# Performance work log

Measured on AMD Instinct MI355X. Metric: run time of the kernel, lower is better.

The kernel has to match this reference:

```python
import jax, jax.numpy as jnp
import numpy as np

N = 100000
E = 1600000
F_IN = 32   # node_features
F_H = 32    # filters
F_OUT = 4


def setup_inputs() -> dict:
    key = jax.random.key(0)
    ks = jax.random.split(key, 24)
    inp = {
        'x': jax.random.normal(ks[0], (N, F_IN), dtype=jnp.float32),
        'edge_index': jax.random.randint(ks[1], (2, E), 0, N, dtype=jnp.int64),
        'edge_weight': jax.random.uniform(ks[2], (E,), dtype=jnp.float32),
        'H': jax.random.normal(ks[3], (N, F_H), dtype=jnp.float32),
    }
    # ChebConv params: W[k] for k in {0,1} (K=2), bias per conv.
    def cheb_params(kw, kb, fin):
        s = 1.0 / np.sqrt(fin)
        W = jax.random.uniform(kw, (2, fin, F_H), jnp.float32, -s, s)
        b = jax.random.uniform(kb, (F_H,), jnp.float32, -s, s)
        return W, b
    names = ['xz', 'hz', 'xr', 'hr', 'xh', 'hh']
    fins = [F_IN, F_H, F_IN, F_H, F_IN, F_H]
    for i, (nm, fin) in enumerate(zip(names, fins)):
        W, b = cheb_params(ks[4 + 2 * i], ks[5 + 2 * i], fin)
        inp['W' + nm] = W
        inp['b' + nm] = b
    s = 1.0 / np.sqrt(F_H)
    inp['lin_w'] = jax.random.uniform(ks[20], (F_H, F_OUT), jnp.float32, -s, s)
    inp['lin_b'] = jax.random.uniform(ks[21], (F_OUT,), jnp.float32, -s, s)
    return inp


def _cheb(x, src, dst, nw, W, b):
    # ChebConv, K=2, sym norm, lambda_max=2 => L_hat = -D^{-1/2} A D^{-1/2}
    # (diagonal of scaled Laplacian cancels exactly: 1 - 1 = 0).
    tx1 = -jax.ops.segment_sum(nw[:, None] * x[src], dst, num_segments=N)
    return x @ W[0] + tx1 @ W[1] + b


def reference(x, edge_index, edge_weight, H,
              Wxz, bxz, Whz, bhz, Wxr, bxr, Whr, bhr, Wxh, bxh, Whh, bhh,
              lin_w, lin_b):
    src, dst = edge_index[0], edge_index[1]
    # remove_self_loops equivalent: zero out self-loop weights
    w = jnp.where(src == dst, 0.0, edge_weight)
    deg = jax.ops.segment_sum(w, src, num_segments=N)
    dinv = jnp.where(deg > 0, jax.lax.rsqrt(jnp.maximum(deg, 1e-30)), 0.0)
    nw = dinv[src] * w * dinv[dst]  # per-edge sym-normalized weight

    Z = jax.nn.sigmoid(_cheb(x, src, dst, nw, Wxz, bxz) +
                       _cheb(H, src, dst, nw, Whz, bhz))
    R = jax.nn.sigmoid(_cheb(x, src, dst, nw, Wxr, bxr) +
                       _cheb(H, src, dst, nw, Whr, bhr))
    H_tilde = jnp.tanh(_cheb(x, src, dst, nw, Wxh, bxh) +
                       _cheb(H * R, src, dst, nw, Whh, bhh))
    h = Z * H + (1.0 - Z) * H_tilde
    out = jax.nn.relu(h) @ lin_w + lin_b
    return (out, h)
```

## Files before the change

kernel.cpp:

```cpp
#include <hip/hip_runtime.h>
#include <hip/hip_bf16.h>
#include <hip/hip_fp16.h>

typedef __hip_bfloat16 bf16;
typedef __attribute__((ext_vector_type(8))) short bf16x8;
typedef __attribute__((ext_vector_type(4))) float f32x4;

#define NN   100000
#define EE   1600000
#define FH   32
#define FOUT 4
#define NBD  782
#define NBS  196
#define CAPB 2432
#define CAPS 8960
#define CAP  64
#define BINBLK 256
#define BINTHR 1024
#define EPB  6250
#define MFMA16(a, b, c) __builtin_amdgcn_mfma_f32_16x16x32_bf16(a, b, c, 0, 0, 0)

__device__ __forceinline__ float b2f(bf16 v) { return __bfloat162float(v); }

__device__ __forceinline__ float ldf(const void* p, int i, int f32) {
    return f32 ? ((const float*)p)[i] : b2f(((const bf16*)p)[i]);
}
__device__ __forceinline__ int ldi(const void* p, int i, int i64f) {
    return i64f ? (int)(((const long long*)p)[i]) : ((const int*)p)[i];
}
__device__ __forceinline__ void stf(void* p, int i, int f32, float v) {
    if (f32) ((float*)p)[i] = v;
    else     ((bf16*)p)[i] = __float2bfloat16(v);
}
__device__ __forceinline__ float h2f(unsigned short u) {
    return __half2float(__ushort_as_half(u));
}
__device__ __forceinline__ unsigned short f2h16(float v) {
    return __half_as_ushort(__float2half(v));
}
__device__ __forceinline__ short f2bf(float v) {
    unsigned u = __float_as_uint(v);
    return (short)((u + 0x7FFFu + ((u >> 16) & 1u)) >> 16);
}
__device__ __forceinline__ unsigned q8(float v) {
    int q = (int)rintf(v * 16.f) + 128;
    q = q < 0 ? 0 : (q > 255 ? 255 : q);
    return (unsigned)q;
}
__device__ __forceinline__ float ub(unsigned w, int k) {
    return (float)((w >> (k * 8)) & 0xFFu);
}
__device__ __forceinline__ float4 bfly_g(float4 v) {
    v.x += __shfl_xor(v.x, 8);  v.y += __shfl_xor(v.y, 8);
    v.z += __shfl_xor(v.z, 8);  v.w += __shfl_xor(v.w, 8);
    v.x += __shfl_xor(v.x, 16); v.y += __shfl_xor(v.y, 16);
    v.z += __shfl_xor(v.z, 16); v.w += __shfl_xor(v.w, 16);
    return v;
}
__device__ __forceinline__ bf16x8 bfragT(const short* __restrict__ wt, int idx) {
    return *(const bf16x8*)(wt + idx);
}

__global__ __launch_bounds__(256) void k_prep(
    const void* __restrict__ x, const void* __restrict__ H,
    const void* __restrict__ ei,
    const void* __restrict__ W0, const void* __restrict__ W1,
    const void* __restrict__ W2, const void* __restrict__ W3,
    const void* __restrict__ W4, const void* __restrict__ W5,
    int* __restrict__ flg, int* __restrict__ binCur, int* __restrict__ binCurS,
    short* __restrict__ wt, unsigned* __restrict__ xh,
    unsigned short* __restrict__ xh8) {
    __shared__ int s_fl[2];
    int t = threadIdx.x, b = blockIdx.x;
    if (t == 0) { s_fl[0] = 0; s_fl[1] = 0; }
    __syncthreads();
    {
        float v = b2f(((const bf16*)x)[t]);
        if ((!isfinite(v)) || (fabsf(v) > 100.f)) atomicOr(&s_fl[0], 1);
        int w32 = ((const int*)ei)[t];
        if ((t & 1) && (w32 != 0)) atomicOr(&s_fl[1], 1);
    }
    __syncthreads();
    int f32 = s_fl[0];
    int i64 = s_fl[1] ? 0 : 1;
    if (b == 0 && t == 0) { flg[0] = f32; flg[1] = i64; }
    if (b < 48) {
        int i = b * 256 + t;
        int mat = i >> 11;
        int r = i & 2047;
        int cheb = r >> 10, k = (r >> 5) & 31, n = r & 31;
        const void* W = (mat == 0) ? W0 : (mat == 1) ? W1 : (mat == 2) ? W2
                      : (mat == 3) ? W3 : (mat == 4) ? W4 : W5;
        wt[(((mat << 1) + cheb) << 10) + n * 32 + k] = f2bf(ldf(W, r, f32));
    } else if (b == 48) {
        for (int i = t; i < NBD; i += 256) binCur[i] = i * CAPB;
    } else if (b == 49) {
        for (int i = t; i < NBS; i += 256) binCurS[i] = i * CAPS;
    }
    int i = b * 256 + t;
    if (i < NN * FH) {
        float xv = ldf(x, i, f32);
        float hv = ldf(H, i, f32);
        xh[i] = ((unsigned)f2h16(hv) << 16) | f2h16(xv);
        xh8[i] = (unsigned short)((q8(hv) << 8) | q8(xv));
    }
}

__global__ __launch_bounds__(BINTHR) void k_bin(const void* __restrict__ ei,
                                                const void* __restrict__ ew,
                                                const int* __restrict__ flg,
                                                int* __restrict__ binCur,
                                                int* __restrict__ binCurS,
                                                int2* __restrict__ dstRec,
                                                int* __restrict__ srcRec) {
    __shared__ int hD[NBD], bD[NBD], lofD[NBD];
    __shared__ int hS[NBS], bS[NBS], lofS[NBS];
    __shared__ int sWave[16];
    __shared__ int2 stD[EPB];
    __shared__ int  stS[EPB];
    int t = threadIdx.x;
    int lane = t & 63, wv = t >> 6;
    for (int i = t; i < NBD; i += BINTHR) hD[i] = 0;
    for (int i = t; i < NBS; i += BINTHR) hS[i] = 0;
    __syncthreads();
    int e0 = blockIdx.x * EPB;
    int e1 = e0 + EPB; if (e1 > EE) e1 = EE;
    int f32 = flg[0], i64 = flg[1];
    for (int e = e0 + t; e < e1; e += BINTHR) {
        int s = ldi(ei, e, i64);
        int d = ldi(ei, EE + e, i64);
        atomicAdd(&hD[d >> 7], 1);
        atomicAdd(&hS[s >> 9], 1);
    }
    __syncthreads();
    for (int i = t; i < NBD; i += BINTHR)
        bD[i] = (hD[i] > 0) ? atomicAdd(&binCur[i], hD[i]) : 0;
    for (int i = t; i < NBS; i += BINTHR)
        bS[i] = (hS[i] > 0) ? atomicAdd(&binCurS[i], hS[i]) : 0;
    int vD = (t < NBD) ? hD[t] : 0;
    int p = vD;
    #pragma unroll
    for (int ofs = 1; ofs < 64; ofs <<= 1) {
        int u = __shfl_up(p, ofs);
        if (lane >= ofs) p += u;
    }
    if (lane == 63) sWave[wv] = p;
    __syncthreads();
    if (t < 16) {
        int q = sWave[t];
        #pragma unroll
        for (int ofs = 1; ofs < 16; ofs <<= 1) {
            int u = __shfl_up(q, ofs);
            if (t >= ofs) q += u;
        }
        sWave[t] = q;
    }
    __syncthreads();
    if (t < NBD) {
        int incl = p + (wv ? sWave[wv - 1] : 0);
        lofD[t] = incl - vD;
        hD[t] = 0;
    }
    __syncthreads();
    int vS = (t < NBS) ? hS[t] : 0;
    p = vS;
    #pragma unroll
    for (int ofs = 1; ofs < 64; ofs <<= 1) {
        int u = __shfl_up(p, ofs);
        if (lane >= ofs) p += u;
    }
    if (lane == 63) sWave[wv] = p;
    __syncthreads();
    if (t < 16) {
        int q = sWave[t];
        #pragma unroll
        for (int ofs = 1; ofs < 16; ofs <<= 1) {
            int u = __shfl_up(q, ofs);
            if (t >= ofs) q += u;
        }
        sWave[t] = q;
    }
    __syncthreads();
    if (t < NBS) {
        int incl = p + (wv ? sWave[wv - 1] : 0);
        lofS[t] = incl - vS;
        hS[t] = 0;
    }
    __syncthreads();
    for (int e = e0 + t; e < e1; e += BINTHR) {
        int s = ldi(ei, e, i64);
        int d = ldi(ei, EE + e, i64);
        float w = (s == d) ? 0.f : ldf(ew, e, f32);
        int wh = (int)(f2h16(w) & 0x7FFFu);
        int bd = d >> 7, bs = s >> 9;
        int rd = atomicAdd(&hD[bd], 1);
        int rs = atomicAdd(&hS[bs], 1);
        stD[lofD[bd] + rd] = make_int2((int)(((unsigned)s << 15) | wh),
                                       (bd << 8) | (d & 127));
        stS[lofS[bs] + rs] = (int)(((unsigned)bs << 24) |
                                   ((unsigned)(s & 511) << 15) | (unsigned)wh);
    }
    __syncthreads();
    int tot = e1 - e0;
    for (int i = t; i < tot; i += BINTHR) {
        int2 r = stD[i];
        int bin = ((unsigned)r.y) >> 8;
        int g = bD[bin] + (i - lofD[bin]);
        if (g < (bin + 1) * CAPB) dstRec[g] = make_int2(r.x, r.y & 127);
        int u = stS[i];
        int sbin = ((unsigned)u) >> 24;
        int gs = bS[sbin] + (i - lofS[sbin]);
        if (gs < (sbin + 1) * CAPS) srcRec[gs] = u & 0xFFFFFF;
    }
}

__global__ __launch_bounds__(256) void k_degb(const int* __restrict__ binCurS,
                                              const int* __restrict__ srcRec,
                                              float* __restrict__ dinv) {
    __shared__ float lDeg[512];
    int b = blockIdx.x, t = threadIdx.x;
    lDeg[t] = 0.f; lDeg[t + 256] = 0.f;
    __syncthreads();
    int cnt = binCurS[b] - b * CAPS;
    if (cnt > CAPS) cnt = CAPS;
    for (int i = t; i < cnt; i += 256) {
        int r = srcRec[b * CAPS + i];
        atomicAdd(&lDeg[(r >> 15) & 511], h2f((unsigned short)(r & 0x7FFF)));
    }
    __syncthreads();
    #pragma unroll
    for (int k = 0; k < 2; k++) {
        int li = t + k * 256;
        int node = b * 512 + li;
        if (node < NN) {
            float dv = lDeg[li];
            dinv[node] = (dv > 0.f) ? rsqrtf(dv) : 0.f;
        }
    }
}

__global__ __launch_bounds__(256) void k_fgz(
    const int* __restrict__ binCur, const int2* __restrict__ dstRec,
    const float* __restrict__ dinv, const unsigned short* __restrict__ xh8,
    const unsigned* __restrict__ xh, const int* __restrict__ flg,
    const short* __restrict__ wt,
    const void* __restrict__ bxz, const void* __restrict__ bhz,
    const void* __restrict__ bxr, const void* __restrict__ bhr,
    int* __restrict__ cursor, int* __restrict__ ell,
    unsigned* __restrict__ axah, unsigned short* __restrict__ zf16,
    unsigned short* __restrict__ hr16) {
    __shared__ int lCur[128];
    __shared__ int lEll[128 * CAP];
    __shared__ unsigned sAX[128][33];
    int b = blockIdx.x, t = threadIdx.x;
    if (t < 128) lCur[t] = 0;
    __syncthreads();
    int cnt = binCur[b] - b * CAPB;
    if (cnt > CAPB) cnt = CAPB;
    for (int i = t; i < cnt; i += 256) {
        int2 r = dstRec[b * CAPB + i];
        int slot = atomicAdd(&lCur[r.y], 1);
        if (slot < CAP) lEll[r.y * CAP + slot] = r.x;
    }
    __syncthreads();
    int nodeBase = b * 128;
    for (int i = t; i < 128 * CAP; i += 256) {
        int node = nodeBase + (i >> 6);
        if (node < NN && (i & 63) < lCur[i >> 6])
            ell[(size_t)node * CAP + (i & 63)] = lEll[i];
    }
    if (t < 128 && nodeBase + t < NN) {
        int c2 = lCur[t]; if (c2 > CAP) c2 = CAP;
        cursor[nodeBase + t] = c2;
    }
    int gg = t >> 5, f = t & 31, g = f >> 3, c = f & 7;
    for (int pass = 0; pass < 16; pass++) {
        int ln = pass * 8 + gg;
        int node = nodeBase + ln;
        if (node >= NN) continue;
        int cnt2 = lCur[ln]; if (cnt2 > CAP) cnt2 = CAP;
        int base = ln * CAP;
        float4 ax = {0.f, 0.f, 0.f, 0.f}, ah = {0.f, 0.f, 0.f, 0.f};
        float cs = 0.f;
        for (int j = 0; j < cnt2; j += 16) {
            int wrd[4]; float cf[4]; uint2 pv[4];
            #pragma unroll
            for (int u = 0; u < 4; u++) {
                int jj = j + u * 4 + g;
                wrd[u] = (jj < cnt2) ? lEll[base + jj] : 0;
            }
            #pragma unroll
            for (int u = 0; u < 4; u++) {
                int s = ((unsigned)wrd[u]) >> 15;
                cf[u] = dinv[s] * h2f((unsigned short)(wrd[u] & 0x7FFF));
                pv[u] = ((const uint2*)xh8)[s * 8 + c];
            }
            #pragma unroll
            for (int u = 0; u < 4; u++) {
                cs += cf[u];
                ax.x += cf[u] * ub(pv[u].x, 0);
                ah.x += cf[u] * ub(pv[u].x, 1);
                ax.y += cf[u] * ub(pv[u].x, 2);
                ah.y += cf[u] * ub(pv[u].x, 3);
                ax.z += cf[u] * ub(pv[u].y, 0);
                ah.z += cf[u] * ub(pv[u].y, 1);
                ax.w += cf[u] * ub(pv[u].y, 2);
                ah.w += cf[u] * ub(pv[u].y, 3);
            }
        }
        ax = bfly_g(ax); ah = bfly_g(ah);
        cs += __shfl_xor(cs, 8);
        cs += __shfl_xor(cs, 16);
        if (g == 0) {
            float dd = -dinv[node];
            float bias = 8.f * cs;
            uint4 o;
            o.x = ((unsigned)f2h16(dd * (ah.x * 0.0625f - bias)) << 16)
                | f2h16(dd * (ax.x * 0.0625f - bias));
            o.y = ((unsigned)f2h16(dd * (ah.y * 0.0625f - bias)) << 16)
                | f2h16(dd * (ax.y * 0.0625f - bias));
            o.z = ((unsigned)f2h16(dd * (ah.z * 0.0625f - bias)) << 16)
                | f2h16(dd * (ax.z * 0.0625f - bias));
            o.w = ((unsigned)f2h16(dd * (ah.w * 0.0625f - bias)) << 16)
                | f2h16(dd * (ax.w * 0.0625f - bias));
            sAX[ln][4 * c + 0] = o.x;
            sAX[ln][4 * c + 1] = o.y;
            sAX[ln][4 * c + 2] = o.z;
            sAX[ln][4 * c + 3] = o.w;
            ((uint4*)(axah + (size_t)node * FH))[c] = o;
        }
    }
    __syncthreads();
    int lane = t & 63, wv = t >> 6;
    int fl32 = flg[0];
    int cc = lane & 15, quad = lane >> 4, kb = quad * 8;
    float bz0 = ldf(bxz, cc, fl32) + ldf(bhz, cc, fl32);
    float bz1 = ldf(bxz, cc + 16, fl32) + ldf(bhz, cc + 16, fl32);
    float br0 = ldf(bxr, cc, fl32) + ldf(bhr, cc, fl32);
    float br1 = ldf(bxr, cc + 16, fl32) + ldf(bhr, cc + 16, fl32);
    for (int half = 0; half < 2; half++) {
        int nb2 = nodeBase + half * 64 + wv * 16;
        int nm = nb2 + cc; if (nm >= NN) nm = NN - 1;
        int lm = nm - nodeBase;
        bf16x8 fx, fHH, fAX, fAH;
        {
            const uint4* p = (const uint4*)(xh + (size_t)nm * FH + kb);
            uint4 aa = p[0], bb = p[1];
            unsigned wd[8] = {aa.x, aa.y, aa.z, aa.w, bb.x, bb.y, bb.z, bb.w};
            #pragma unroll
            for (int j = 0; j < 8; j++) {
                fx[j]  = f2bf(h2f((unsigned short)(wd[j] & 0xFFFF)));
                fHH[j] = f2bf(h2f((unsigned short)(wd[j] >> 16)));
            }
        }
        {
            unsigned wd[8];
            #pragma unroll
            for (int j = 0; j < 8; j++) wd[j] = sAX[lm][kb + j];
            #pragma unroll
            for (int j = 0; j < 8; j++) {
                fAX[j] = f2bf(h2f((unsigned short)(wd[j] & 0xFFFF)));
                fAH[j] = f2bf(h2f((unsigned short)(wd[j] >> 16)));
            }
        }
        f32x4 az0 = {bz0, bz0, bz0, bz0}, az1 = {bz1, bz1, bz1, bz1};
        f32x4 ar0 = {br0, br0, br0, br0}, ar1 = {br1, br1, br1, br1};
        int i0 = cc * 32 + kb;
        int i1 = (cc + 16) * 32 + kb;
        az0 = MFMA16(fx,  bfragT(wt, 0 * 1024 + i0), az0);
        az0 = MFMA16(fAX, bfragT(wt, 1 * 1024 + i0), az0);
        az0 = MFMA16(fHH, bfragT(wt, 2 * 1024 + i0), az0);
        az0 = MFMA16(fAH, bfragT(wt, 3 * 1024 + i0), az0);
        az1 = MFMA16(fx,  bfragT(wt, 0 * 1024 + i1), az1);
        az1 = MFMA16(fAX, bfragT(wt, 1 * 1024 + i1), az1);
        az1 = MFMA16(fHH, bfragT(wt, 2 * 1024 + i1), az1);
        az1 = MFMA16(fAH, bfragT(wt, 3 * 1024 + i1), az1);
        ar0 = MFMA16(fx,  bfragT(wt, 4 * 1024 + i0), ar0);
        ar0 = MFMA16(fAX, bfragT(wt, 5 * 1024 + i0), ar0);
        ar0 = MFMA16(fHH, bfragT(wt, 6 * 1024 + i0), ar0);
        ar0 = MFMA16(fAH, bfragT(wt, 7 * 1024 + i0), ar0);
        ar1 = MFMA16(fx,  bfragT(wt, 4 * 1024 + i1), ar1);
        ar1 = MFMA16(fAX, bfragT(wt, 5 * 1024 + i1), ar1);
        ar1 = MFMA16(fHH, bfragT(wt, 6 * 1024 + i1), ar1);
        ar1 = MFMA16(fAH, bfragT(wt, 7 * 1024 + i1), ar1);
        #pragma unroll
        for (int tl = 0; tl < 2; tl++) {
            f32x4 az = tl ? az1 : az0, ar = tl ? ar1 : ar0;
            int ff = cc + 16 * tl;
            #pragma unroll
            for (int r = 0; r < 4; r++) {
                int node = nb2 + quad * 4 + r;
                if (node < NN) {
                    float zv = 1.f / (1.f + expf(-az[r]));
                    float rv = 1.f / (1.f + expf(-ar[r]));
                    float Hv = h2f((unsigned short)(xh[(size_t)node * FH + ff] >> 16));
                    zf16[(size_t)node * FH + ff] = f2h16(zv);
                    hr16[(size_t)node * FH + ff] = f2h16(Hv * rv);
                }
            }
        }
    }
}

__global__ __launch_bounds__(256) void k_fgf(
    const int* __restrict__ cursor, const int* __restrict__ ell,
    const float* __restrict__ dinv, const unsigned short* __restrict__ hr16,
    const unsigned* __restrict__ xh, const unsigned* __restrict__ axah,
    const int* __restrict__ flg, const short* __restrict__ wt,
    const unsigned short* __restrict__ zf16,
    const void* __restrict__ bxh, const void* __restrict__ bhh,
    const void* __restrict__ lin_w, const void* __restrict__ lin_b,
    void* __restrict__ out) {
    __shared__ unsigned sAHR[64][17];
    __shared__ float srh[64][FH];
    __shared__ float slw[FH * FOUT];
    __shared__ float slb[FOUT];
    int b = blockIdx.x, t = threadIdx.x;
    int f32 = flg[0];
    if (t < FH * FOUT) slw[t] = ldf(lin_w, t, f32);
    if (t < FOUT) slb[t] = ldf(lin_b, t, f32);
    int nodeBase = b * 64;
    int gg = t >> 5, f = t & 31, g = f >> 3, c = f & 7;
    for (int pass = 0; pass < 8; pass++) {
        int ln = pass * 8 + gg;
        int node = nodeBase + ln;
        if (node >= NN) continue;
        int cnt = cursor[node];
        size_t base = (size_t)node * CAP;
        float4 acc = {0.f, 0.f, 0.f, 0.f};
        for (int j = 0; j < cnt; j += 16) {
            int wrd[4]; float cf[4]; ushort4 hv[4];
            #pragma unroll
            for (int u = 0; u < 4; u++) {
                int jj = j + u * 4 + g;
                wrd[u] = (jj < cnt) ? ell[base + jj] : 0;
            }
            #pragma unroll
            for (int u = 0; u < 4; u++) {
                int s = ((unsigned)wrd[u]) >> 15;
                cf[u] = dinv[s] * h2f((unsigned short)(wrd[u] & 0x7FFF));
                hv[u] = ((const ushort4*)hr16)[s * 8 + c];
            }
            #pragma unroll
            for (int u = 0; u < 4; u++) {
                acc.x += cf[u] * h2f(hv[u].x);
                acc.y += cf[u] * h2f(hv[u].y);
                acc.z += cf[u] * h2f(hv[u].z);
                acc.w += cf[u] * h2f(hv[u].w);
            }
        }
        acc = bfly_g(acc);
        if (g == 0) {
            float dd = -dinv[node];
            sAHR[ln][2 * c + 0] = ((unsigned)f2h16(dd * acc.y) << 16)
                                | f2h16(dd * acc.x);
            sAHR[ln][2 * c + 1] = ((unsigned)f2h16(dd * acc.w) << 16)
                                | f2h16(dd * acc.z);
        }
    }
    __syncthreads();
    int lane = t & 63, wv = t >> 6;
    int cc = lane & 15, quad = lane >> 4, kb = quad * 8;
    int nb2 = nodeBase + wv * 16;
    int nm = nb2 + cc; if (nm >= NN) nm = NN - 1;
    int lm = nm - nodeBase;
    bf16x8 fx, fAX, fHR, fAHR;
    {
        const uint4* p = (const uint4*)(xh + (size_t)nm * FH + kb);
        uint4 aa = p[0], bb = p[1];
        unsigned wd[8] = {aa.x, aa.y, aa.z, aa.w, bb.x, bb.y, bb.z, bb.w};
        #pragma unroll
        for (int j = 0; j < 8; j++)
            fx[j] = f2bf(h2f((unsigned short)(wd[j] & 0xFFFF)));
    }
    {
        const uint4* p = (const uint4*)(axah + (size_t)nm * FH + kb);
        uint4 aa = p[0], bb = p[1];
        unsigned wd[8] = {aa.x, aa.y, aa.z, aa.w, bb.x, bb.y, bb.z, bb.w};
        #pragma unroll
        for (int j = 0; j < 8; j++)
            fAX[j] = f2bf(h2f((unsigned short)(wd[j] & 0xFFFF)));
    }
    {
        const uint4* p = (const uint4*)(hr16 + (size_t)nm * FH + kb);
        uint4 aa = p[0];
        unsigned wd[4] = {aa.x, aa.y, aa.z, aa.w};
        #pragma unroll
        for (int j = 0; j < 8; j++)
            fHR[j] = f2bf(h2f((unsigned short)((wd[j >> 1] >> ((j & 1) * 16)) & 0xFFFF)));
    }
    {
        unsigned wd[4];
        #pragma unroll
        for (int m = 0; m < 4; m++) wd[m] = sAHR[lm][kb / 2 + m];
        #pragma unroll
        for (int j = 0; j < 8; j++)
            fAHR[j] = f2bf(h2f((unsigned short)((wd[j >> 1] >> ((j & 1) * 16)) & 0xFFFF)));
    }
    float bh0 = ldf(bxh, cc, f32) + ldf(bhh, cc, f32);
    float bh1 = ldf(bxh, cc + 16, f32) + ldf(bhh, cc + 16, f32);
    f32x4 a0 = {bh0, bh0, bh0, bh0}, a1 = {bh1, bh1, bh1, bh1};
    int i0 = cc * 32 + kb;
    int i1 = (cc + 16) * 32 + kb;
    a0 = MFMA16(fx,   bfragT(wt,  8 * 1024 + i0), a0);
    a0 = MFMA16(fAX,  bfragT(wt,  9 * 1024 + i0), a0);
    a0 = MFMA16(fHR,  bfragT(wt, 10 * 1024 + i0), a0);
    a0 = MFMA16(fAHR, bfragT(wt, 11 * 1024 + i0), a0);
    a1 = MFMA16(fx,   bfragT(wt,  8 * 1024 + i1), a1);
    a1 = MFMA16(fAX,  bfragT(wt,  9 * 1024 + i1), a1);
    a1 = MFMA16(fHR,  bfragT(wt, 10 * 1024 + i1), a1);
    a1 = MFMA16(fAHR, bfragT(wt, 11 * 1024 + i1), a1);
    #pragma unroll
    for (int tl = 0; tl < 2; tl++) {
        f32x4 a = tl ? a1 : a0;
        int ff = cc + 16 * tl;
        #pragma unroll
        for (int r = 0; r < 4; r++) {
            int node = nb2 + quad * 4 + r;
            if (node < NN) {
                float ht = tanhf(a[r]);
                float zv = h2f(zf16[(size_t)node * FH + ff]);
                float Hv = h2f((unsigned short)(xh[(size_t)node * FH + ff] >> 16));
                float hval = zv * Hv + (1.f - zv) * ht;
                stf(out, NN * FOUT + node * FH + ff, f32, hval);
                srh[node - nodeBase][ff] = hval > 0.f ? hval : 0.f;
            }
        }
    }
    __syncthreads();
    int nl = t >> 2, fo = t & 3;
    int node2 = nodeBase + nl;
    if (node2 < NN) {
        float acc = slb[fo];
        #pragma unroll
        for (int k = 0; k < FH; k++) acc += srh[nl][k] * slw[k * FOUT + fo];
        stf(out, node2 * FOUT + fo, f32, acc);
    }
}

extern "C" void kernel_launch(void* const* d_in, const int* in_sizes, int n_in,
                              void* d_out, int out_size, void* d_ws, size_t ws_size,
                              hipStream_t stream) {
    const void* x   = d_in[0];
    const void* ei  = d_in[1];
    const void* ew  = d_in[2];
    const void* H   = d_in[3];
    const void* Wxz = d_in[4];
    const void* bxz = d_in[5];
    const void* Whz = d_in[6];
    const void* bhz = d_in[7];
    const void* Wxr = d_in[8];
    const void* bxr = d_in[9];
    const void* Whr = d_in[10];
    const void* bhr = d_in[11];
    const void* Wxh = d_in[12];
    const void* bxh = d_in[13];
    const void* Whh = d_in[14];
    const void* bhh = d_in[15];
    const void* lnw = d_in[16];
    const void* lnb = d_in[17];

    char* base = (char*)d_ws;
    int*            flg     = (int*)base;            base += 64;
    int*            binCur  = (int*)base;            base += (NBD * 4 + 63) & ~63;
    int*            binCurS = (int*)base;            base += (NBS * 4 + 63) & ~63;
    float*          dinv    = (float*)base;          base += (size_t)NN * 4;
    int*            cursor  = (int*)base;            base += (size_t)NN * 4;
    short*          wt      = (short*)base;          base += (12288 * 2 + 63) & ~63;
    unsigned*       xh      = (unsigned*)base;       base += (size_t)NN * FH * 4;
    unsigned short* xh8     = (unsigned short*)base; base += (size_t)NN * FH * 2;
    unsigned*       axah    = (unsigned*)base;       base += (size_t)NN * FH * 4;
    unsigned short* zf16    = (unsigned short*)base; base += (size_t)NN * FH * 2;
    unsigned short* hr16    = (unsigned short*)base; base += (size_t)NN * FH * 2;
    int*            ell     = (int*)base;            base += (size_t)NN * CAP * 4;
    int2*           dstRec  = (int2*)base;           base += (size_t)NBD * CAPB * 8;
    int*            srcRec  = (int*)base;

    const int pb   = (NN * FH + 255) / 256;
    const int n64b = (NN + 63) / 64;

    k_prep<<<pb, 256, 0, stream>>>(x, H, ei, Wxz, Whz, Wxr, Whr, Wxh, Whh,
                                   flg, binCur, binCurS, wt, xh, xh8);
    k_bin<<<BINBLK, BINTHR, 0, stream>>>(ei, ew, flg, binCur, binCurS,
                                         dstRec, srcRec);
    k_degb<<<NBS, 256, 0, stream>>>(binCurS, srcRec, dinv);
    k_fgz<<<NBD, 256, 0, stream>>>(binCur, dstRec, dinv, xh8, xh, flg, wt,
                                   bxz, bhz, bxr, bhr,
                                   cursor, ell, axah, zf16, hr16);
    k_fgf<<<n64b, 256, 0, stream>>>(cursor, ell, dinv, hr16, xh, axah, flg, wt,
                                    zf16, bxh, bhh, lnw, lnb, d_out);
}
```

Measured before the change: 292.7 us.

## Split fused ELL-fill/gather/MFMA kernel into three separate kernels

Breaks the fused k_fgz kernel into three kernels: one that builds the ELL adjacency from binned records, one gather kernel with 8 nodes per block over many more blocks, and one MFMA kernel that computes the Z and R gates. The aim is more parallelism and occupancy for the gather, which previously used large shared memory and ran 16 serial passes per block. In exchange the gather now reads ELL from global memory instead of LDS, there are two extra kernel launches, and axah makes an extra round trip through global memory.

```diff
diff --git a/kernel.cpp b/kernel.cpp
--- a/kernel.cpp
+++ b/kernel.cpp
@@ -214,6 +214,35 @@
     }
 }
 
+__global__ __launch_bounds__(256) void k_fillb(const int* __restrict__ binCur,
+                                               const int2* __restrict__ dstRec,
+                                               int* __restrict__ cursor,
+                                               int* __restrict__ ell) {
+    __shared__ int lCur[128];
+    __shared__ int lEll[128 * CAP];
+    int b = blockIdx.x, t = threadIdx.x;
+    if (t < 128) lCur[t] = 0;
+    __syncthreads();
+    int cnt = binCur[b] - b * CAPB;
+    if (cnt > CAPB) cnt = CAPB;
+    for (int i = t; i < cnt; i += 256) {
+        int2 r = dstRec[b * CAPB + i];
+        int slot = atomicAdd(&lCur[r.y], 1);
+        if (slot < CAP) lEll[r.y * CAP + slot] = r.x;
+    }
+    __syncthreads();
+    int nodeBase = b * 128;
+    for (int i = t; i < 128 * CAP; i += 256) {
+        int node = nodeBase + (i >> 6);
+        if (node < NN && (i & 63) < lCur[i >> 6])
+            ell[(size_t)node * CAP + (i & (CAP - 1))] = lEll[i];
+    }
+    if (t < 128 && nodeBase + t < NN) {
+        int c = lCur[t]; if (c > CAP) c = CAP;
+        cursor[nodeBase + t] = c;
+    }
+}
+
 __global__ __launch_bounds__(256) void k_degb(const int* __restrict__ binCurS,
                                               const int* __restrict__ srcRec,
                                               float* __restrict__ dinv) {
@@ -239,164 +268,139 @@
     }
 }
 
-__global__ __launch_bounds__(256) void k_fgz(
-    const int* __restrict__ binCur, const int2* __restrict__ dstRec,
-    const float* __restrict__ dinv, const unsigned short* __restrict__ xh8,
-    const unsigned* __restrict__ xh, const int* __restrict__ flg,
-    const short* __restrict__ wt,
+__global__ __launch_bounds__(256) void k_gather1(const int* __restrict__ cursor,
+                                                 const int* __restrict__ ell,
+                                                 const float* __restrict__ dinv,
+                                                 const unsigned short* __restrict__ xh8,
+                                                 unsigned* __restrict__ axah) {
+    int t = threadIdx.x;
+    int node = blockIdx.x * 8 + (t >> 5);
+    if (node >= NN) return;
+    int f = t & 31;
+    int g = f >> 3, c = f & 7;
+    int cnt = cursor[node];
+    size_t base = (size_t)node * CAP;
+    float4 ax = {0.f, 0.f, 0.f, 0.f}, ah = {0.f, 0.f, 0.f, 0.f};
+    float cs = 0.f;
+    for (int j = 0; j < cnt; j += 16) {
+        int wrd[4]; float cf[4]; uint2 pv[4];
+        #pragma unroll
+        for (int u = 0; u < 4; u++) {
+            int jj = j + u * 4 + g;
+            wrd[u] = (jj < cnt) ? ell[base + jj] : 0;
+        }
+        #pragma unroll
+        for (int u = 0; u < 4; u++) {
+            int s = ((unsigned)wrd[u]) >> 15;
+            cf[u] = dinv[s] * h2f((unsigned short)(wrd[u] & 0x7FFF));
+            pv[u] = ((const uint2*)xh8)[s * 8 + c];
+        }
+        #pragma unroll
+        for (int u = 0; u < 4; u++) {
+            cs += cf[u];
+            ax.x += cf[u] * ub(pv[u].x, 0);
+            ah.x += cf[u] * ub(pv[u].x, 1);
+            ax.y += cf[u] * ub(pv[u].x, 2);
+            ah.y += cf[u] * ub(pv[u].x, 3);
+            ax.z += cf[u] * ub(pv[u].y, 0);
+            ah.z += cf[u] * ub(pv[u].y, 1);
+            ax.w += cf[u] * ub(pv[u].y, 2);
+            ah.w += cf[u] * ub(pv[u].y, 3);
+        }
+    }
+    ax = bfly_g(ax); ah = bfly_g(ah);
+    cs += __shfl_xor(cs, 8);
+    cs += __shfl_xor(cs, 16);
+    if (g == 0) {
+        float dd = -dinv[node];
+        float bias = 8.f * cs;
+        uint4 o;
+        o.x = ((unsigned)f2h16(dd * (ah.x * 0.0625f - bias)) << 16)
+            | f2h16(dd * (ax.x * 0.0625f - bias));
+        o.y = ((unsigned)f2h16(dd * (ah.y * 0.0625f - bias)) << 16)
+            | f2h16(dd * (ax.y * 0.0625f - bias));
+        o.z = ((unsigned)f2h16(dd * (ah.z * 0.0625f - bias)) << 16)
+            | f2h16(dd * (ax.z * 0.0625f - bias));
+        o.w = ((unsigned)f2h16(dd * (ah.w * 0.0625f - bias)) << 16)
+            | f2h16(dd * (ax.w * 0.0625f - bias));
+        ((uint4*)(axah + (size_t)node * FH))[c] = o;
+    }
+}
+
+__global__ __launch_bounds__(256) void k_zr_mfma(
+    const unsigned* __restrict__ xh, const unsigned* __restrict__ axah,
+    const int* __restrict__ flg, const short* __restrict__ wt,
     const void* __restrict__ bxz, const void* __restrict__ bhz,
     const void* __restrict__ bxr, const void* __restrict__ bhr,
-    int* __restrict__ cursor, int* __restrict__ ell,
-    unsigned* __restrict__ axah, unsigned short* __restrict__ zf16,
-    unsigned short* __restrict__ hr16) {
-    __shared__ int lCur[128];
-    __shared__ int lEll[128 * CAP];
-    __shared__ unsigned sAX[128][33];
-    int b = blockIdx.x, t = threadIdx.x;
-    if (t < 128) lCur[t] = 0;
-    __syncthreads();
-    int cnt = binCur[b] - b * CAPB;
-    if (cnt > CAPB) cnt = CAPB;
-    for (int i = t; i < cnt; i += 256) {
-        int2 r = dstRec[b * CAPB + i];
-        int slot = atomicAdd(&lCur[r.y], 1);
-        if (slot < CAP) lEll[r.y * CAP + slot] = r.x;
-    }
-    __syncthreads();
-    int nodeBase = b * 128;
-    for (int i = t; i < 128 * CAP; i += 256) {
-        int node = nodeBase + (i >> 6);
-        if (node < NN && (i & 63) < lCur[i >> 6])
-            ell[(size_t)node * CAP + (i & 63)] = lEll[i];
-    }
-    if (t < 128 && nodeBase + t < NN) {
-        int c2 = lCur[t]; if (c2 > CAP) c2 = CAP;
-        cursor[nodeBase + t] = c2;
-    }
-    int gg = t >> 5, f = t & 31, g = f >> 3, c = f & 7;
-    for (int pass = 0; pass < 16; pass++) {
-        int ln = pass * 8 + gg;
-        int node = nodeBase + ln;
-        if (node >= NN) continue;
-        int cnt2 = lCur[ln]; if (cnt2 > CAP) cnt2 = CAP;
-        int base = ln * CAP;
-        float4 ax = {0.f, 0.f, 0.f, 0.f}, ah = {0.f, 0.f, 0.f, 0.f};
-        float cs = 0.f;
-        for (int j = 0; j < cnt2; j += 16) {
-            int wrd[4]; float cf[4]; uint2 pv[4];
-            #pragma unroll
-            for (int u = 0; u < 4; u++) {
-                int jj = j + u * 4 + g;
-                wrd[u] = (jj < cnt2) ? lEll[base + jj] : 0;
-            }
-            #pragma unroll
-            for (int u = 0; u < 4; u++) {
-                int s = ((unsigned)wrd[u]) >> 15;
-                cf[u] = dinv[s] * h2f((unsigned short)(wrd[u] & 0x7FFF));
-                pv[u] = ((const uint2*)xh8)[s * 8 + c];
-            }
-            #pragma unroll
-            for (int u = 0; u < 4; u++) {
-                cs += cf[u];
-                ax.x += cf[u] * ub(pv[u].x, 0);
-                ah.x += cf[u] * ub(pv[u].x, 1);
-                ax.y += cf[u] * ub(pv[u].x, 2);
-                ah.y += cf[u] * ub(pv[u].x, 3);
-                ax.z += cf[u] * ub(pv[u].y, 0);
-                ah.z += cf[u] * ub(pv[u].y, 1);
-                ax.w += cf[u] * ub(pv[u].y, 2);
-                ah.w += cf[u] * ub(pv[u].y, 3);
-            }
-        }
-        ax = bfly_g(ax); ah = bfly_g(ah);
-        cs += __shfl_xor(cs, 8);
-        cs += __shfl_xor(cs, 16);
-        if (g == 0) {
-            float dd = -dinv[node];
-            float bias = 8.f * cs;
-            uint4 o;
-            o.x = ((unsigned)f2h16(dd * (ah.x * 0.0625f - bias)) << 16)
-                | f2h16(dd * (ax.x * 0.0625f - bias));
-            o.y = ((unsigned)f2h16(dd * (ah.y * 0.0625f - bias)) << 16)
-                | f2h16(dd * (ax.y * 0.0625f - bias));
-            o.z = ((unsigned)f2h16(dd * (ah.z * 0.0625f - bias)) << 16)
-                | f2h16(dd * (ax.z * 0.0625f - bias));
-            o.w = ((unsigned)f2h16(dd * (ah.w * 0.0625f - bias)) << 16)
-                | f2h16(dd * (ax.w * 0.0625f - bias));
-            sAX[ln][4 * c + 0] = o.x;
-            sAX[ln][4 * c + 1] = o.y;
-            sAX[ln][4 * c + 2] = o.z;
-            sAX[ln][4 * c + 3] = o.w;
-            ((uint4*)(axah + (size_t)node * FH))[c] = o;
-        }
-    }
-    __syncthreads();
+    unsigned short* __restrict__ zf16, unsigned short* __restrict__ hr16) {
+    int t = threadIdx.x;
     int lane = t & 63, wv = t >> 6;
-    int fl32 = flg[0];
-    int cc = lane & 15, quad = lane >> 4, kb = quad * 8;
-    float bz0 = ldf(bxz, cc, fl32) + ldf(bhz, cc, fl32);
-    float bz1 = ldf(bxz, cc + 16, fl32) + ldf(bhz, cc + 16, fl32);
-    float br0 = ldf(bxr, cc, fl32) + ldf(bhr, cc, fl32);
-    float br1 = ldf(bxr, cc + 16, fl32) + ldf(bhr, cc + 16, fl32);
-    for (int half = 0; half < 2; half++) {
-        int nb2 = nodeBase + half * 64 + wv * 16;
-        int nm = nb2 + cc; if (nm >= NN) nm = NN - 1;
-        int lm = nm - nodeBase;
-        bf16x8 fx, fHH, fAX, fAH;
-        {
-            const uint4* p = (const uint4*)(xh + (size_t)nm * FH + kb);
-            uint4 aa = p[0], bb = p[1];
-            unsigned wd[8] = {aa.x, aa.y, aa.z, aa.w, bb.x, bb.y, bb.z, bb.w};
-            #pragma unroll
-            for (int j = 0; j < 8; j++) {
-                fx[j]  = f2bf(h2f((unsigned short)(wd[j] & 0xFFFF)));
-                fHH[j] = f2bf(h2f((unsigned short)(wd[j] >> 16)));
-            }
-        }
-        {
-            unsigned wd[8];
-            #pragma unroll
-            for (int j = 0; j < 8; j++) wd[j] = sAX[lm][kb + j];
-            #pragma unroll
-            for (int j = 0; j < 8; j++) {
-                fAX[j] = f2bf(h2f((unsigned short)(wd[j] & 0xFFFF)));
-                fAH[j] = f2bf(h2f((unsigned short)(wd[j] >> 16)));
-            }
-        }
-        f32x4 az0 = {bz0, bz0, bz0, bz0}, az1 = {bz1, bz1, bz1, bz1};
-        f32x4 ar0 = {br0, br0, br0, br0}, ar1 = {br1, br1, br1, br1};
-        int i0 = cc * 32 + kb;
-        int i1 = (cc + 16) * 32 + kb;
-        az0 = MFMA16(fx,  bfragT(wt, 0 * 1024 + i0), az0);
-        az0 = MFMA16(fAX, bfragT(wt, 1 * 1024 + i0), az0);
-        az0 = MFMA16(fHH, bfragT(wt, 2 * 1024 + i0), az0);
-        az0 = MFMA16(fAH, bfragT(wt, 3 * 1024 + i0), az0);
-        az1 = MFMA16(fx,  bfragT(wt, 0 * 1024 + i1), az1);
-        az1 = MFMA16(fAX, bfragT(wt, 1 * 1024 + i1), az1);
-        az1 = MFMA16(fHH, bfragT(wt, 2 * 1024 + i1), az1);
-        az1 = MFMA16(fAH, bfragT(wt, 3 * 1024 + i1), az1);
-        ar0 = MFMA16(fx,  bfragT(wt, 4 * 1024 + i0), ar0);
-        ar0 = MFMA16(fAX, bfragT(wt, 5 * 1024 + i0), ar0);
-        ar0 = MFMA16(fHH, bfragT(wt, 6 * 1024 + i0), ar0);
-        ar0 = MFMA16(fAH, bfragT(wt, 7 * 1024 + i0), ar0);
-        ar1 = MFMA16(fx,  bfragT(wt, 4 * 1024 + i1), ar1);
-        ar1 = MFMA16(fAX, bfragT(wt, 5 * 1024 + i1), ar1);
-        ar1 = MFMA16(fHH, bfragT(wt, 6 * 1024 + i1), ar1);
-        ar1 = MFMA16(fAH, bfragT(wt, 7 * 1024 + i1), ar1);
-        #pragma unroll
-        for (int tl = 0; tl < 2; tl++) {
-            f32x4 az = tl ? az1 : az0, ar = tl ? ar1 : ar0;
-            int ff = cc + 16 * tl;
-            #pragma unroll
-            for (int r = 0; r < 4; r++) {
-                int node = nb2 + quad * 4 + r;
-                if (node < NN) {
-                    float zv = 1.f / (1.f + expf(-az[r]));
-                    float rv = 1.f / (1.f + expf(-ar[r]));
-                    float Hv = h2f((unsigned short)(xh[(size_t)node * FH + ff] >> 16));
-                    zf16[(size_t)node * FH + ff] = f2h16(zv);
-                    hr16[(size_t)node * FH + ff] = f2h16(Hv * rv);
-                }
+    int f32 = flg[0];
+    int c = lane & 15, quad = lane >> 4, kb = quad * 8;
+    int nodeBase = blockIdx.x * 64 + wv * 16;
+    int nm = nodeBase + c; if (nm >= NN) nm = NN - 1;
+
+    bf16x8 fx, fHH, fAX, fAH;
+    {
+        const uint4* p = (const uint4*)(xh + (size_t)nm * FH + kb);
+        uint4 a = p[0], b = p[1];
+        unsigned wd[8] = {a.x, a.y, a.z, a.w, b.x, b.y, b.z, b.w};
+        #pragma unroll
+        for (int j = 0; j < 8; j++) {
+            fx[j]  = f2bf(h2f((unsigned short)(wd[j] & 0xFFFF)));
+            fHH[j] = f2bf(h2f((unsigned short)(wd[j] >> 16)));
+        }
+    }
+    {
+        const uint4* p = (const uint4*)(axah + (size_t)nm * FH + kb);
+        uint4 a = p[0], b = p[1];
+        unsigned wd[8] = {a.x, a.y, a.z, a.w, b.x, b.y, b.z, b.w};
+        #pragma unroll
+        for (int j = 0; j < 8; j++) {
+            fAX[j] = f2bf(h2f((unsigned short)(wd[j] & 0xFFFF)));
+            fAH[j] = f2bf(h2f((unsigned short)(wd[j] >> 16)));
+        }
+    }
+
+    float bz0 = ldf(bxz, c, f32) + ldf(bhz, c, f32);
+    float bz1 = ldf(bxz, c + 16, f32) + ldf(bhz, c + 16, f32);
+    float br0 = ldf(bxr, c, f32) + ldf(bhr, c, f32);
+    float br1 = ldf(bxr, c + 16, f32) + ldf(bhr, c + 16, f32);
+    f32x4 az0 = {bz0, bz0, bz0, bz0}, az1 = {bz1, bz1, bz1, bz1};
+    f32x4 ar0 = {br0, br0, br0, br0}, ar1 = {br1, br1, br1, br1};
+
+    int i0 = c * 32 + kb;
+    int i1 = (c + 16) * 32 + kb;
+    az0 = MFMA16(fx,  bfragT(wt, 0 * 1024 + i0), az0);
+    az0 = MFMA16(fAX, bfragT(wt, 1 * 1024 + i0), az0);
+    az0 = MFMA16(fHH, bfragT(wt, 2 * 1024 + i0), az0);
+    az0 = MFMA16(fAH, bfragT(wt, 3 * 1024 + i0), az0);
+    az1 = MFMA16(fx,  bfragT(wt, 0 * 1024 + i1), az1);
+    az1 = MFMA16(fAX, bfragT(wt, 1 * 1024 + i1), az1);
+    az1 = MFMA16(fHH, bfragT(wt, 2 * 1024 + i1), az1);
+    az1 = MFMA16(fAH, bfragT(wt, 3 * 1024 + i1), az1);
+    ar0 = MFMA16(fx,  bfragT(wt, 4 * 1024 + i0), ar0);
+    ar0 = MFMA16(fAX, bfragT(wt, 5 * 1024 + i0), ar0);
+    ar0 = MFMA16(fHH, bfragT(wt, 6 * 1024 + i0), ar0);
+    ar0 = MFMA16(fAH, bfragT(wt, 7 * 1024 + i0), ar0);
+    ar1 = MFMA16(fx,  bfragT(wt, 4 * 1024 + i1), ar1);
+    ar1 = MFMA16(fAX, bfragT(wt, 5 * 1024 + i1), ar1);
+    ar1 = MFMA16(fHH, bfragT(wt, 6 * 1024 + i1), ar1);
+    ar1 = MFMA16(fAH, bfragT(wt, 7 * 1024 + i1), ar1);
+
+    #pragma unroll
+    for (int tl = 0; tl < 2; tl++) {
+        f32x4 az = tl ? az1 : az0, ar = tl ? ar1 : ar0;
+        int f = c + 16 * tl;
+        #pragma unroll
+        for (int r = 0; r < 4; r++) {
+            int node = nodeBase + quad * 4 + r;
+            if (node < NN) {
+                float zv = 1.f / (1.f + expf(-az[r]));
+                float rv = 1.f / (1.f + expf(-ar[r]));
+                float Hv = h2f((unsigned short)(xh[(size_t)node * FH + f] >> 16));
+                zf16[(size_t)node * FH + f] = f2h16(zv);
+                hr16[(size_t)node * FH + f] = f2h16(Hv * rv);
             }
         }
     }
@@ -577,16 +581,18 @@
     int*            srcRec  = (int*)base;
 
     const int pb   = (NN * FH + 255) / 256;
+    const int n8b  = (NN + 7) / 8;
     const int n64b = (NN + 63) / 64;
 
     k_prep<<<pb, 256, 0, stream>>>(x, H, ei, Wxz, Whz, Wxr, Whr, Wxh, Whh,
                                    flg, binCur, binCurS, wt, xh, xh8);
     k_bin<<<BINBLK, BINTHR, 0, stream>>>(ei, ew, flg, binCur, binCurS,
                                          dstRec, srcRec);
+    k_fillb<<<NBD, 256, 0, stream>>>(binCur, dstRec, cursor, ell);
     k_degb<<<NBS, 256, 0, stream>>>(binCurS, srcRec, dinv);
-    k_fgz<<<NBD, 256, 0, stream>>>(binCur, dstRec, dinv, xh8, xh, flg, wt,
-                                   bxz, bhz, bxr, bhr,
-                                   cursor, ell, axah, zf16, hr16);
+    k_gather1<<<n8b, 256, 0, stream>>>(cursor, ell, dinv, xh8, axah);
+    k_zr_mfma<<<n64b, 256, 0, stream>>>(xh, axah, flg, wt,
+                                        bxz, bhz, bxr, bhr, zf16, hr16);
     k_fgf<<<n64b, 256, 0, stream>>>(cursor, ell, dinv, hr16, xh, axah, flg, wt,
                                     zf16, bxh, bhh, lnw, lnb, d_out);
 }
```

After: 272.0 us. 1.08x faster.
